# Kernel tuning notes

Measured on AMD Instinct MI355X. Metric: run time of the kernel, lower is better.

Reference implementation:

```python
import jax, jax.numpy as jnp
import numpy as np

B, L, DF = 1024, 64, 2048
E, U, V = 256, 512, 32000
BN_EPS = 1e-3  # keras BatchNormalization default epsilon


def setup_inputs() -> dict:
    key = jax.random.key(0)
    ks = jax.random.split(key, 16)
    s = lambda *sh: 1.0 / np.sqrt(sh[0])
    return {
        "tokens": jax.random.randint(ks[0], (B, 1), 0, V),
        "featureMap": jax.random.normal(ks[1], (B, L, DF), jnp.float32),
        "prevState": jax.random.normal(ks[2], (B, U), jnp.float32),
        "emb": jax.random.normal(ks[3], (V, E), jnp.float32) * 0.05,
        "Wu": jax.random.normal(ks[4], (DF, U), jnp.float32) * s(DF),
        "bu": jnp.zeros((U,), jnp.float32),
        "Ww": jax.random.normal(ks[5], (U, U), jnp.float32) * s(U),
        "bw": jnp.zeros((U,), jnp.float32),
        "Wv": jax.random.normal(ks[6], (U, 1), jnp.float32) * s(U),
        "bv": jnp.zeros((1,), jnp.float32),
        "gru_k": jax.random.normal(ks[7], (DF + E, 3 * U), jnp.float32) * s(DF + E),
        "gru_rk": jax.random.normal(ks[8], (U, 3 * U), jnp.float32) * s(U),
        "gru_b": jnp.zeros((2, 3 * U), jnp.float32),
        "W1": jax.random.normal(ks[9], (U, U), jnp.float32) * s(U),
        "b1": jnp.zeros((U,), jnp.float32),
        "gamma": jnp.ones((U,), jnp.float32),
        "beta": jnp.zeros((U,), jnp.float32),
        "mmean": jnp.zeros((U,), jnp.float32),
        "mvar": jnp.ones((U,), jnp.float32),
        "W2": jax.random.normal(ks[10], (U, V), jnp.float32) * s(U),
        "b2": jnp.zeros((V,), jnp.float32),
    }


def reference(tokens, featureMap, prevState, emb, Wu, bu, Ww, bw, Wv, bv,
              gru_k, gru_rk, gru_b, W1, b1, gamma, beta, mmean, mvar, W2, b2):
    u = gru_rk.shape[0]
    # Bahdanau attention: score over L pixel positions
    state = prevState[:, None, :]                                   # [B,1,U]
    score = jnp.tanh(featureMap @ Wu + bu + state @ Ww + bw) @ Wv + bv  # [B,L,1]
    attn = jax.nn.softmax(score, axis=1)                            # [B,L,1]
    ctx = jnp.sum(attn * featureMap, axis=1)                        # [B,DF]
    # embedding lookup + concat context
    ex = emb[tokens]                                                # [B,1,E]
    x = jnp.concatenate([ctx[:, None, :], ex], axis=-1)[:, 0, :]    # [B,DF+E]
    # single-step GRU (keras reset_after=True), initial state = zeros
    xg = x @ gru_k + gru_b[0]                                       # [B,3U]
    rg = gru_b[1]                                                   # h0=0 -> recurrent term is just bias
    z = jax.nn.sigmoid(xg[:, :u] + rg[:u])
    r = jax.nn.sigmoid(xg[:, u:2 * u] + rg[u:2 * u])
    hh = jnp.tanh(xg[:, 2 * u:] + r * rg[2 * u:])
    h = (1.0 - z) * hh                                              # z*h0 + (1-z)*hh, h0=0
    # dense -> dropout(eval: identity) -> batchnorm(inference) -> dense
    y = h @ W1 + b1
    y = (y - mmean) * jax.lax.rsqrt(mvar + BN_EPS) * gamma + beta
    logits = y @ W2 + b2                                            # [B,V]
    return logits, h, attn
```

## Files before the change

### kernel.cpp

```cpp
#include <hip/hip_runtime.h>

typedef unsigned short u16;
typedef unsigned int   u32;
typedef __attribute__((ext_vector_type(8))) short short8;
typedef __attribute__((ext_vector_type(4))) float f32x4;

#define DEV static __device__ __forceinline__

DEV u16 f2bf(float f){
  union { float f; u32 u; } v; v.f = f;
  u32 u = v.u;
  u += 0x7fffu + ((u >> 16) & 1u);
  return (u16)(u >> 16);
}
DEV float sigmoidf_(float x){ return 1.f / (1.f + __expf(-x)); }
DEV float tanh_fast(float x){ float e = __expf(2.f * x); return 1.f - 2.f / (e + 1.f); }

DEV void gload16(const void* g, void* l){
  __builtin_amdgcn_global_load_lds(
      (const __attribute__((address_space(1))) void*)g,
      (__attribute__((address_space(3))) void*)l, 16, 0, 0);
}
DEV f32x4 mfma16(short8 a, short8 b, f32x4 c){
  return __builtin_amdgcn_mfma_f32_16x16x32_bf16(a, b, c, 0, 0, 0);
}

__global__ __launch_bounds__(256) void k_transpose_cvt(
    const float* __restrict__ src, u16* __restrict__ dst, int K, int N){
  __shared__ u16 t[64][72];
  int k0 = blockIdx.x << 6, n0 = blockIdx.y << 6;
  int tid = threadIdx.x;
  int r = tid >> 2, c0 = (tid & 3) << 4;
#pragma unroll
  for (int i = 0; i < 4; i++){
    float4 v = *(const float4*)&src[(size_t)(k0 + r) * N + n0 + c0 + i * 4];
    *(u32*)&t[r][c0 + i * 4 + 0] = (u32)f2bf(v.x) | ((u32)f2bf(v.y) << 16);
    *(u32*)&t[r][c0 + i * 4 + 2] = (u32)f2bf(v.z) | ((u32)f2bf(v.w) << 16);
  }
  __syncthreads();
  int n = tid >> 2, cc = (tid & 3) << 4;
  union { u16 s[16]; uint4 q[2]; } pk;
#pragma unroll
  for (int i = 0; i < 16; i++) pk.s[i] = t[cc + i][n];
  uint4* o = (uint4*)(dst + (size_t)(n0 + n) * K + k0 + cc);
  o[0] = pk.q[0]; o[1] = pk.q[1];
}

__global__ __launch_bounds__(512) void k_q(
    const float* __restrict__ ps, const float* __restrict__ Ww,
    const float* __restrict__ bw, const float* __restrict__ bu,
    float* __restrict__ q){
  __shared__ float psl[16][512];
  int b0 = blockIdx.x << 4;
  int tid = threadIdx.x;
#pragma unroll
  for (int i = 0; i < 16; i++) psl[i][tid] = ps[(size_t)(b0 + i) * 512 + tid];
  __syncthreads();
  float acc[16];
#pragma unroll
  for (int i = 0; i < 16; i++) acc[i] = 0.f;
  for (int j = 0; j < 512; j++){
    float w = Ww[(size_t)j * 512 + tid];
#pragma unroll
    for (int i = 0; i < 16; i++) acc[i] = fmaf(psl[i][j], w, acc[i]);
  }
  float bias = bw[tid] + bu[tid];
#pragma unroll
  for (int i = 0; i < 16; i++) q[(size_t)(b0 + i) * 512 + tid] = acc[i] + bias;
}

__global__ __launch_bounds__(256) void k_gather(
    const int* __restrict__ tok, const float* __restrict__ emb, u16* __restrict__ xbf){
  int b = blockIdx.x, e = threadIdx.x;
  int t = tok[b];
  xbf[(size_t)b * 2304 + 2048 + e] = f2bf(emb[(size_t)t * 256 + e]);
}

__global__ __launch_bounds__(512) void k_bnprep(
    const float* __restrict__ gamma, const float* __restrict__ beta,
    const float* __restrict__ mmean, const float* __restrict__ mvar,
    const float* __restrict__ b1, float* __restrict__ bns, float* __restrict__ bno){
  int u = threadIdx.x;
  float sc = gamma[u] * rsqrtf(mvar[u] + 1e-3f);
  bns[u] = sc;
  bno[u] = (b1[u] - mmean[u]) * sc + beta[u];
}

__global__ __launch_bounds__(512, 4) void k_attn(
    const float* __restrict__ fm, const u16* __restrict__ WuT,
    const float* __restrict__ q, const float* __restrict__ Wv,
    float* __restrict__ attn_out, u16* __restrict__ xbf){
  __shared__ __align__(16) u16 Al[2 * 64 * 64];
  __shared__ float qv[512], wvv[512];
  __shared__ float scoreBuf[8][64];
  __shared__ float attn_s[64];

  int b = blockIdx.x;
  int tid = threadIdx.x, wid = tid >> 6, lane = tid & 63;
  qv[tid] = q[(size_t)b * 512 + tid];
  wvv[tid] = Wv[tid];
  const float* fmb = fm + (size_t)b * (64 * 2048);

  f32x4 acc[4][4];
#pragma unroll
  for (int i = 0; i < 4; i++)
#pragma unroll
    for (int j = 0; j < 4; j++) acc[i][j] = (f32x4){0.f, 0.f, 0.f, 0.f};

  int arow = tid >> 3, ac = tid & 7;
  int asl = ac ^ (arow & 7);
  const float* gaBase = fmb + (size_t)arow * 2048 + ac * 8;

  const u16* bp[4];
#pragma unroll
  for (int ni = 0; ni < 4; ni++)
    bp[ni] = WuT + (size_t)(wid * 64 + ni * 16 + (lane & 15)) * 2048 + ((lane >> 4) << 3);

  auto writeA = [&](int buf, float4 v0, float4 v1){
    union { u16 s[8]; uint4 q; } pk;
    pk.s[0] = f2bf(v0.x); pk.s[1] = f2bf(v0.y); pk.s[2] = f2bf(v0.z); pk.s[3] = f2bf(v0.w);
    pk.s[4] = f2bf(v1.x); pk.s[5] = f2bf(v1.y); pk.s[6] = f2bf(v1.z); pk.s[7] = f2bf(v1.w);
    *(uint4*)&Al[buf * 4096 + arow * 64 + asl * 8] = pk.q;
  };

  {
    float4 v0 = *(const float4*)gaBase;
    float4 v1 = *(const float4*)(gaBase + 4);
    writeA(0, v0, v1);
  }
  __syncthreads();

  int cur = 0;
  for (int t = 0; t < 32; t++){
    float4 v0, v1;
    if (t < 31){
      const float* ga = gaBase + ((t + 1) << 6);
      v0 = *(const float4*)ga;
      v1 = *(const float4*)(ga + 4);
    }
#pragma unroll
    for (int kh = 0; kh < 2; kh++){
      short8 af[4], bfr[4];
#pragma unroll
      for (int ni = 0; ni < 4; ni++)
        bfr[ni] = *(const short8*)(bp[ni] + (t << 6) + (kh << 5));
#pragma unroll
      for (int mi = 0; mi < 4; mi++){
        int r = mi * 16 + (lane & 15);
        af[mi] = *(const short8*)&Al[cur * 4096 + r * 64 + (((kh << 2) + (lane >> 4)) ^ (r & 7)) * 8];
      }
#pragma unroll
      for (int mi = 0; mi < 4; mi++)
#pragma unroll
        for (int ni = 0; ni < 4; ni++)
          acc[mi][ni] = mfma16(af[mi], bfr[ni], acc[mi][ni]);
    }
    if (t < 31) writeA(cur ^ 1, v0, v1);
    __syncthreads();
    cur ^= 1;
  }

  float part[16];
#pragma unroll
  for (int mi = 0; mi < 4; mi++)
#pragma unroll
    for (int j = 0; j < 4; j++){
      float s = 0.f;
#pragma unroll
      for (int ni = 0; ni < 4; ni++){
        int u = wid * 64 + ni * 16 + (lane & 15);
        s += tanh_fast(acc[mi][ni][j] + qv[u]) * wvv[u];
      }
      part[mi * 4 + j] = s;
    }
#pragma unroll
  for (int i = 0; i < 16; i++){
    part[i] += __shfl_xor(part[i], 1);
    part[i] += __shfl_xor(part[i], 2);
    part[i] += __shfl_xor(part[i], 4);
    part[i] += __shfl_xor(part[i], 8);
  }
  if ((lane & 15) == 0){
    int g = lane >> 4;
#pragma unroll
    for (int mi = 0; mi < 4; mi++)
#pragma unroll
      for (int j = 0; j < 4; j++)
        scoreBuf[wid][mi * 16 + g * 4 + j] = part[mi * 4 + j];
  }
  __syncthreads();
  if (tid < 64){
    float s = 0.f;
#pragma unroll
    for (int w = 0; w < 8; w++) s += scoreBuf[w][tid];
    float mx = s;
#pragma unroll
    for (int m = 32; m >= 1; m >>= 1) mx = fmaxf(mx, __shfl_xor(mx, m));
    float e = __expf(s - mx);
    float sum = e;
#pragma unroll
    for (int m = 32; m >= 1; m >>= 1) sum += __shfl_xor(sum, m);
    float a = e / sum;
    attn_s[tid] = a;
    attn_out[(size_t)b * 64 + tid] = a;
  }
  __syncthreads();
  const float4* fmr = (const float4*)fmb;
  float4 cx = {0.f, 0.f, 0.f, 0.f};
  for (int l = 0; l < 64; l++){
    float a = attn_s[l];
    float4 v = fmr[l * 512 + tid];
    cx.x = fmaf(a, v.x, cx.x); cx.y = fmaf(a, v.y, cx.y);
    cx.z = fmaf(a, v.z, cx.z); cx.w = fmaf(a, v.w, cx.w);
  }
  uint2 o;
  o.x = (u32)f2bf(cx.x) | ((u32)f2bf(cx.y) << 16);
  o.y = (u32)f2bf(cx.z) | ((u32)f2bf(cx.w) << 16);
  *(uint2*)&xbf[(size_t)b * 2304 + tid * 4] = o;
}

template<bool OBF>
__global__ __launch_bounds__(512) void k_gemm(
    const u16* __restrict__ A, const u16* __restrict__ Bt,
    const float* __restrict__ scale, const float* __restrict__ off,
    void* __restrict__ Cout, int K, int N){
  __shared__ __align__(16) u16 Alds[2][128 * 64];
  __shared__ __align__(16) u16 Blds[2][128 * 64];
  int n0 = blockIdx.x << 7, m0 = blockIdx.y << 7;
  int tid = threadIdx.x, wid = tid >> 6, lane = tid & 63;
  int wm = wid >> 2, wn = wid & 3;

  f32x4 acc[4][2];
#pragma unroll
  for (int i = 0; i < 4; i++)
#pragma unroll
    for (int j = 0; j < 2; j++) acc[i][j] = (f32x4){0.f, 0.f, 0.f, 0.f};

  auto stage = [&](int s, int k0){
#pragma unroll
    for (int i = 0; i < 2; i++){
      int p = ((wid * 2 + i) << 6) + lane;
      int row = p >> 3, sl = p & 7, sl2 = sl ^ (row & 7);
      gload16(A  + (size_t)(m0 + row) * K + k0 + sl2 * 8,
              (char*)Alds[s] + (size_t)(wid * 2 + i) * 1024);
      gload16(Bt + (size_t)(n0 + row) * K + k0 + sl2 * 8,
              (char*)Blds[s] + (size_t)(wid * 2 + i) * 1024);
    }
  };

  int nk = K >> 6;
  stage(0, 0);
  __syncthreads();
  int cur = 0;
  for (int t = 0; t < nk; t++){
    if (t + 1 < nk) stage(cur ^ 1, (t + 1) << 6);
#pragma unroll
    for (int kh = 0; kh < 2; kh++){
      short8 af[4], bfr[2];
#pragma unroll
      for (int mi = 0; mi < 4; mi++){
        int r = wm * 64 + mi * 16 + (lane & 15);
        af[mi] = *(const short8*)&Alds[cur][r * 64 + (((kh << 2) + (lane >> 4)) ^ (r & 7)) * 8];
      }
#pragma unroll
      for (int ni = 0; ni < 2; ni++){
        int r = wn * 32 + ni * 16 + (lane & 15);
        bfr[ni] = *(const short8*)&Blds[cur][r * 64 + (((kh << 2) + (lane >> 4)) ^ (r & 7)) * 8];
      }
#pragma unroll
      for (int mi = 0; mi < 4; mi++)
#pragma unroll
        for (int ni = 0; ni < 2; ni++)
          acc[mi][ni] = mfma16(af[mi], bfr[ni], acc[mi][ni]);
    }
    __syncthreads();
    cur ^= 1;
  }
#pragma unroll
  for (int ni = 0; ni < 2; ni++){
    int n = n0 + wn * 32 + ni * 16 + (lane & 15);
    float sc = scale ? scale[n] : 1.f;
    float of = off ? off[n] : 0.f;
#pragma unroll
    for (int mi = 0; mi < 4; mi++)
#pragma unroll
      for (int j = 0; j < 4; j++){
        int m = m0 + wm * 64 + mi * 16 + (lane >> 4) * 4 + j;
        float v = acc[mi][ni][j] * sc + of;
        if (OBF) ((u16*)Cout)[(size_t)m * N + n] = f2bf(v);
        else     ((float*)Cout)[(size_t)m * N + n] = v;
      }
  }
}

__global__ __launch_bounds__(512) void k_gates(
    const float* __restrict__ xg, const float* __restrict__ gru_b,
    float* __restrict__ hout, u16* __restrict__ hbf){
  int b = blockIdx.x, u = threadIdx.x;
  const float* rg = gru_b + 1536;
  size_t base = (size_t)b * 1536;
  float z  = sigmoidf_(xg[base + u]        + rg[u]);
  float r  = sigmoidf_(xg[base + 512 + u]  + rg[512 + u]);
  float hh = tanh_fast(xg[base + 1024 + u] + r * rg[1024 + u]);
  float h = (1.f - z) * hh;
  hout[(size_t)b * 512 + u] = h;
  hbf[(size_t)b * 512 + u] = f2bf(h);
}

extern "C" void kernel_launch(void* const* d_in, const int* in_sizes, int n_in,
                              void* d_out, int out_size, void* d_ws, size_t ws_size,
                              hipStream_t stream){
  const int*   tok   = (const int*)  d_in[0];
  const float* fm    = (const float*)d_in[1];
  const float* ps    = (const float*)d_in[2];
  const float* emb   = (const float*)d_in[3];
  const float* Wu    = (const float*)d_in[4];
  const float* bu    = (const float*)d_in[5];
  const float* Ww    = (const float*)d_in[6];
  const float* bw    = (const float*)d_in[7];
  const float* Wv    = (const float*)d_in[8];
  const float* gru_k = (const float*)d_in[10];
  const float* gru_b = (const float*)d_in[12];
  const float* W1    = (const float*)d_in[13];
  const float* b1    = (const float*)d_in[14];
  const float* gamma = (const float*)d_in[15];
  const float* beta  = (const float*)d_in[16];
  const float* mmean = (const float*)d_in[17];
  const float* mvar  = (const float*)d_in[18];
  const float* W2    = (const float*)d_in[19];
  const float* b2    = (const float*)d_in[20];

  float* logits = (float*)d_out;
  float* hout   = (float*)d_out + 32768000;
  float* attn   = (float*)d_out + 33292288;

  char* ws = (char*)d_ws;
  u16*   WuT = (u16*)  (ws + 0);
  u16*   gkT = (u16*)  (ws + 2097152);
  u16*   W2T = (u16*)  (ws + 9175040);
  u16*   W1T = (u16*)  (ws + 41943040);
  float* qws = (float*)(ws + 42467328);
  u16*   xbf = (u16*)  (ws + 44564480);
  float* xg  = (float*)(ws + 49283072);
  u16*   hbf = (u16*)  (ws + 55574528);
  u16*   ybf = (u16*)  (ws + 56623104);
  float* bns = (float*)(ws + 57671680);
  float* bno = (float*)(ws + 57673728);

  k_transpose_cvt<<<dim3(32, 8),  256, 0, stream>>>(Wu,    WuT, 2048, 512);
  k_transpose_cvt<<<dim3(36, 24), 256, 0, stream>>>(gru_k, gkT, 2304, 1536);
  k_transpose_cvt<<<dim3(8, 500), 256, 0, stream>>>(W2,    W2T, 512,  32000);
  k_transpose_cvt<<<dim3(8, 8),   256, 0, stream>>>(W1,    W1T, 512,  512);
  k_q<<<64, 512, 0, stream>>>(ps, Ww, bw, bu, qws);
  k_gather<<<1024, 256, 0, stream>>>(tok, emb, xbf);
  k_bnprep<<<1, 512, 0, stream>>>(gamma, beta, mmean, mvar, b1, bns, bno);
  k_attn<<<1024, 512, 0, stream>>>(fm, WuT, qws, Wv, attn, xbf);
  k_gemm<false><<<dim3(12, 8), 512, 0, stream>>>(xbf, gkT, nullptr, gru_b, xg, 2304, 1536);
  k_gates<<<1024, 512, 0, stream>>>(xg, gru_b, hout, hbf);
  k_gemm<true><<<dim3(4, 8), 512, 0, stream>>>(hbf, W1T, bns, bno, ybf, 512, 512);
  k_gemm<false><<<dim3(250, 8), 512, 0, stream>>>(ybf, W2T, nullptr, b2, logits, 512, 32000);
}
```

Measured before the change: 593.6 us.

## Split attention into tiled score GEMM, softmax, and context kernels

Replaces the per-batch fused attention kernel with three kernels. The first is a 128x128 tiled score GEMM that stages WuT through LDS with global-to-LDS loads and writes partial scores for each of four column blocks. A small softmax kernel sums those partials, and a separate context kernel computes the attention-weighted sum. This aims for better MFMA tile shapes and shared staging of B. The cost is that the fp32 featureMap is read and converted once per column block (four times), plus an extra pass for the context, which adds memory traffic unless caches absorb it.

```diff
diff --git a/kernel.cpp b/kernel.cpp
--- a/kernel.cpp
+++ b/kernel.cpp
@@ -86,130 +86,152 @@
   bno[u] = (b1[u] - mmean[u]) * sc + beta[u];
 }
 
-__global__ __launch_bounds__(512, 4) void k_attn(
+__global__ __launch_bounds__(512, 4) void k_score_gemm(
     const float* __restrict__ fm, const u16* __restrict__ WuT,
     const float* __restrict__ q, const float* __restrict__ Wv,
-    float* __restrict__ attn_out, u16* __restrict__ xbf){
-  __shared__ __align__(16) u16 Al[2 * 64 * 64];
-  __shared__ float qv[512], wvv[512];
-  __shared__ float scoreBuf[8][64];
-  __shared__ float attn_s[64];
-
-  int b = blockIdx.x;
+    float* __restrict__ sp){
+  __shared__ __align__(16) u16 Alds[2][128 * 64];
+  __shared__ __align__(16) u16 Blds[2][128 * 64];
+  __shared__ float qsl[2][128], wvsl[128];
+  __shared__ float part[128][4];
+
+  int bid = blockIdx.x;
+  int slab = bid >> 2, nblk = bid & 3;
+  int n0 = nblk << 7;
+  size_t gm0 = (size_t)slab << 7;
   int tid = threadIdx.x, wid = tid >> 6, lane = tid & 63;
-  qv[tid] = q[(size_t)b * 512 + tid];
-  wvv[tid] = Wv[tid];
-  const float* fmb = fm + (size_t)b * (64 * 2048);
-
-  f32x4 acc[4][4];
+  int wm = wid >> 2, wn = wid & 3;
+
+  if (tid < 256) qsl[tid >> 7][tid & 127] = q[(size_t)((slab << 1) + (tid >> 7)) * 512 + n0 + (tid & 127)];
+  else if (tid < 384) wvsl[tid - 256] = Wv[n0 + (tid - 256)];
+
+  f32x4 acc[4][2];
 #pragma unroll
   for (int i = 0; i < 4; i++)
 #pragma unroll
-    for (int j = 0; j < 4; j++) acc[i][j] = (f32x4){0.f, 0.f, 0.f, 0.f};
-
-  int arow = tid >> 3, ac = tid & 7;
-  int asl = ac ^ (arow & 7);
-  const float* gaBase = fmb + (size_t)arow * 2048 + ac * 8;
-
-  const u16* bp[4];
-#pragma unroll
-  for (int ni = 0; ni < 4; ni++)
-    bp[ni] = WuT + (size_t)(wid * 64 + ni * 16 + (lane & 15)) * 2048 + ((lane >> 4) << 3);
-
-  auto writeA = [&](int buf, float4 v0, float4 v1){
-    union { u16 s[8]; uint4 q; } pk;
-    pk.s[0] = f2bf(v0.x); pk.s[1] = f2bf(v0.y); pk.s[2] = f2bf(v0.z); pk.s[3] = f2bf(v0.w);
-    pk.s[4] = f2bf(v1.x); pk.s[5] = f2bf(v1.y); pk.s[6] = f2bf(v1.z); pk.s[7] = f2bf(v1.w);
-    *(uint4*)&Al[buf * 4096 + arow * 64 + asl * 8] = pk.q;
+    for (int j = 0; j < 2; j++) acc[i][j] = (f32x4){0.f, 0.f, 0.f, 0.f};
+
+  int arow = tid >> 2, ac = (tid & 3) << 1;
+  const float* gaBase = fm + (gm0 + arow) * 2048 + ac * 8;
+  int asl0 = (ac ^ (arow & 7)) * 8, asl1 = ((ac + 1) ^ (arow & 7)) * 8;
+
+  auto stageB = [&](int s, int k0){
+#pragma unroll
+    for (int i = 0; i < 2; i++){
+      int p = ((wid * 2 + i) << 6) + lane;
+      int row = p >> 3, sl = p & 7, sl2 = sl ^ (row & 7);
+      gload16(WuT + (size_t)(n0 + row) * 2048 + k0 + sl2 * 8,
+              (char*)Blds[s] + (size_t)(wid * 2 + i) * 1024);
+    }
   };
-
+  auto cvtWriteA = [&](int s, float4 a0, float4 a1, float4 a2, float4 a3){
+    union { u16 w[8]; uint4 q; } p0, p1;
+    p0.w[0]=f2bf(a0.x); p0.w[1]=f2bf(a0.y); p0.w[2]=f2bf(a0.z); p0.w[3]=f2bf(a0.w);
+    p0.w[4]=f2bf(a1.x); p0.w[5]=f2bf(a1.y); p0.w[6]=f2bf(a1.z); p0.w[7]=f2bf(a1.w);
+    p1.w[0]=f2bf(a2.x); p1.w[1]=f2bf(a2.y); p1.w[2]=f2bf(a2.z); p1.w[3]=f2bf(a2.w);
+    p1.w[4]=f2bf(a3.x); p1.w[5]=f2bf(a3.y); p1.w[6]=f2bf(a3.z); p1.w[7]=f2bf(a3.w);
+    *(uint4*)&Alds[s][arow * 64 + asl0] = p0.q;
+    *(uint4*)&Alds[s][arow * 64 + asl1] = p1.q;
+  };
+
+  stageB(0, 0);
   {
-    float4 v0 = *(const float4*)gaBase;
-    float4 v1 = *(const float4*)(gaBase + 4);
-    writeA(0, v0, v1);
+    float4 a0 = *(const float4*)(gaBase + 0);
+    float4 a1 = *(const float4*)(gaBase + 4);
+    float4 a2 = *(const float4*)(gaBase + 8);
+    float4 a3 = *(const float4*)(gaBase + 12);
+    cvtWriteA(0, a0, a1, a2, a3);
   }
   __syncthreads();
 
   int cur = 0;
   for (int t = 0; t < 32; t++){
-    float4 v0, v1;
+    float4 a0, a1, a2, a3;
     if (t < 31){
+      stageB(cur ^ 1, (t + 1) << 6);
       const float* ga = gaBase + ((t + 1) << 6);
-      v0 = *(const float4*)ga;
-      v1 = *(const float4*)(ga + 4);
+      a0 = *(const float4*)(ga + 0);
+      a1 = *(const float4*)(ga + 4);
+      a2 = *(const float4*)(ga + 8);
+      a3 = *(const float4*)(ga + 12);
     }
 #pragma unroll
     for (int kh = 0; kh < 2; kh++){
-      short8 af[4], bfr[4];
-#pragma unroll
-      for (int ni = 0; ni < 4; ni++)
-        bfr[ni] = *(const short8*)(bp[ni] + (t << 6) + (kh << 5));
+      short8 af[4], bfr[2];
 #pragma unroll
       for (int mi = 0; mi < 4; mi++){
-        int r = mi * 16 + (lane & 15);
-        af[mi] = *(const short8*)&Al[cur * 4096 + r * 64 + (((kh << 2) + (lane >> 4)) ^ (r & 7)) * 8];
+        int r = wm * 64 + mi * 16 + (lane & 15);
+        af[mi] = *(const short8*)&Alds[cur][r * 64 + (((kh << 2) + (lane >> 4)) ^ (r & 7)) * 8];
+      }
+#pragma unroll
+      for (int ni = 0; ni < 2; ni++){
+        int r = wn * 32 + ni * 16 + (lane & 15);
+        bfr[ni] = *(const short8*)&Blds[cur][r * 64 + (((kh << 2) + (lane >> 4)) ^ (r & 7)) * 8];
       }
 #pragma unroll
       for (int mi = 0; mi < 4; mi++)
 #pragma unroll
-        for (int ni = 0; ni < 4; ni++)
+        for (int ni = 0; ni < 2; ni++)
           acc[mi][ni] = mfma16(af[mi], bfr[ni], acc[mi][ni]);
     }
-    if (t < 31) writeA(cur ^ 1, v0, v1);
+    if (t < 31) cvtWriteA(cur ^ 1, a0, a1, a2, a3);
     __syncthreads();
     cur ^= 1;
   }
 
-  float part[16];
 #pragma unroll
   for (int mi = 0; mi < 4; mi++)
 #pragma unroll
     for (int j = 0; j < 4; j++){
+      int bloc = (wm * 64 + mi * 16 + (lane >> 4) * 4 + j) >> 6;
       float s = 0.f;
 #pragma unroll
-      for (int ni = 0; ni < 4; ni++){
-        int u = wid * 64 + ni * 16 + (lane & 15);
-        s += tanh_fast(acc[mi][ni][j] + qv[u]) * wvv[u];
-      }
-      part[mi * 4 + j] = s;
-    }
-#pragma unroll
-  for (int i = 0; i < 16; i++){
-    part[i] += __shfl_xor(part[i], 1);
-    part[i] += __shfl_xor(part[i], 2);
-    part[i] += __shfl_xor(part[i], 4);
-    part[i] += __shfl_xor(part[i], 8);
-  }
-  if ((lane & 15) == 0){
-    int g = lane >> 4;
-#pragma unroll
-    for (int mi = 0; mi < 4; mi++)
-#pragma unroll
-      for (int j = 0; j < 4; j++)
-        scoreBuf[wid][mi * 16 + g * 4 + j] = part[mi * 4 + j];
-  }
-  __syncthreads();
-  if (tid < 64){
-    float s = 0.f;
-#pragma unroll
-    for (int w = 0; w < 8; w++) s += scoreBuf[w][tid];
-    float mx = s;
-#pragma unroll
-    for (int m = 32; m >= 1; m >>= 1) mx = fmaxf(mx, __shfl_xor(mx, m));
-    float e = __expf(s - mx);
-    float sum = e;
-#pragma unroll
-    for (int m = 32; m >= 1; m >>= 1) sum += __shfl_xor(sum, m);
-    float a = e / sum;
-    attn_s[tid] = a;
-    attn_out[(size_t)b * 64 + tid] = a;
-  }
-  __syncthreads();
-  const float4* fmr = (const float4*)fmb;
+      for (int ni = 0; ni < 2; ni++){
+        int ul = wn * 32 + ni * 16 + (lane & 15);
+        s += tanh_fast(acc[mi][ni][j] + qsl[bloc][ul]) * wvsl[ul];
+      }
+      s += __shfl_xor(s, 1);
+      s += __shfl_xor(s, 2);
+      s += __shfl_xor(s, 4);
+      s += __shfl_xor(s, 8);
+      if ((lane & 15) == 0)
+        part[wm * 64 + mi * 16 + (lane >> 4) * 4 + j][wn] = s;
+    }
+  __syncthreads();
+  if (tid < 128){
+    float s = part[tid][0] + part[tid][1] + part[tid][2] + part[tid][3];
+    sp[(size_t)nblk * 65536 + gm0 + tid] = s;
+  }
+}
+
+__global__ __launch_bounds__(64) void k_softmax(
+    const float* __restrict__ sp, float* __restrict__ attn_out){
+  int b = blockIdx.x, l = threadIdx.x;
+  size_t m = (size_t)b * 64 + l;
+  float s = sp[m] + sp[65536 + m] + sp[2 * 65536 + m] + sp[3 * 65536 + m];
+  float mx = s;
+#pragma unroll
+  for (int k = 32; k >= 1; k >>= 1) mx = fmaxf(mx, __shfl_xor(mx, k));
+  float e = __expf(s - mx);
+  float sum = e;
+#pragma unroll
+  for (int k = 32; k >= 1; k >>= 1) sum += __shfl_xor(sum, k);
+  attn_out[m] = e / sum;
+}
+
+__global__ __launch_bounds__(512) void k_ctx(
+    const float* __restrict__ fm, const float* __restrict__ attn,
+    u16* __restrict__ xbf){
+  __shared__ float as_[64];
+  int b = blockIdx.x, tid = threadIdx.x;
+  if (tid < 64) as_[tid] = attn[(size_t)b * 64 + tid];
+  __syncthreads();
+  const float4* fmr = (const float4*)(fm + (size_t)b * (64 * 2048));
   float4 cx = {0.f, 0.f, 0.f, 0.f};
+#pragma unroll 4
   for (int l = 0; l < 64; l++){
-    float a = attn_s[l];
-    float4 v = fmr[l * 512 + tid];
+    float a = as_[l];
+    float4 v = fmr[(size_t)l * 512 + tid];
     cx.x = fmaf(a, v.x, cx.x); cx.y = fmaf(a, v.y, cx.y);
     cx.z = fmaf(a, v.z, cx.z); cx.w = fmaf(a, v.w, cx.w);
   }
@@ -346,6 +368,7 @@
   u16*   ybf = (u16*)  (ws + 56623104);
   float* bns = (float*)(ws + 57671680);
   float* bno = (float*)(ws + 57673728);
+  float* sp  = xg;
 
   k_transpose_cvt<<<dim3(32, 8),  256, 0, stream>>>(Wu,    WuT, 2048, 512);
   k_transpose_cvt<<<dim3(36, 24), 256, 0, stream>>>(gru_k, gkT, 2304, 1536);
@@ -354,7 +377,9 @@
   k_q<<<64, 512, 0, stream>>>(ps, Ww, bw, bu, qws);
   k_gather<<<1024, 256, 0, stream>>>(tok, emb, xbf);
   k_bnprep<<<1, 512, 0, stream>>>(gamma, beta, mmean, mvar, b1, bns, bno);
-  k_attn<<<1024, 512, 0, stream>>>(fm, WuT, qws, Wv, attn, xbf);
+  k_score_gemm<<<2048, 512, 0, stream>>>(fm, WuT, qws, Wv, sp);
+  k_softmax<<<1024, 64, 0, stream>>>(sp, attn);
+  k_ctx<<<1024, 512, 0, stream>>>(fm, attn, xbf);
   k_gemm<false><<<dim3(12, 8), 512, 0, stream>>>(xbf, gkT, nullptr, gru_b, xg, 2304, 1536);
   k_gates<<<1024, 512, 0, stream>>>(xg, gru_b, hout, hbf);
   k_gemm<true><<<dim3(4, 8), 512, 0, stream>>>(hbf, W1T, bns, bno, ybf, 512, 512);
```

Measured after the change: 850.6 us. 1.43x slower.
